# Performance work log

Measured on AMD Instinct MI355X. Metric: run time of the kernel, lower is better.

Reference implementation:

```python
import jax, jax.numpy as jnp
import numpy as np

NUM_ELMT = 64
INPUT_DIM = 16
BOUND = 50.0
MESH_RATIO = 1.2
N_POINTS = 1_048_576


def _build_mesh():
    m = NUM_ELMT
    one_step = BOUND * (MESH_RATIO - 1.0) / (MESH_RATIO ** (m / 2) - 1.0)
    idx = np.arange(-m / 2, m / 2 + 1)
    mesh = (MESH_RATIO ** np.abs(idx) - 1.0) / (MESH_RATIO - 1.0) * one_step * np.sign(idx)
    mesh_norm = (mesh + BOUND) / (2.0 * BOUND)
    mesh_norm = np.concatenate([[0.0], mesh_norm[1:-1], [1.0]]).astype(np.float32)
    elmt_size = (mesh_norm[1:] - mesh_norm[:-1]).astype(np.float32)
    return jnp.asarray(mesh_norm), jnp.asarray(elmt_size)


def setup_inputs() -> dict:
    key = jax.random.key(0)
    k1, k2 = jax.random.split(key)
    x = jax.random.uniform(k1, (N_POINTS, INPUT_DIM), jnp.float32, minval=-BOUND, maxval=BOUND)
    pdj = jnp.ones((N_POINTS, 1), jnp.float32)
    sldj = jnp.zeros((N_POINTS, 1), jnp.float32)
    log_p = 0.1 * jax.random.normal(k2, (NUM_ELMT - 1, INPUT_DIM), jnp.float32)
    mesh_norm, elmt_size = _build_mesh()
    return {"x": x, "pdj": pdj, "sldj": sldj, "log_p": log_p,
            "mesh_norm": mesh_norm, "elmt_size": elmt_size}


def _normalize_pdf(log_p, elmt_size):
    # elmt_size: (M,) -> (M,1) column, log_p: (M-1, D)
    es = elmt_size[:, None]
    ep = jnp.exp(log_p)
    px = ep * (es[:-1] + es[1:]) / 2.0
    px = ep * (1.0 - es[0]) / jnp.sum(px, axis=0, keepdims=True)
    p0 = jnp.ones((1, log_p.shape[1]), log_p.dtype)
    pdf_norm = jnp.concatenate([p0, px, p0], axis=0)            # (M+1, D)
    cell = (pdf_norm[:-1] + pdf_norm[1:]) / 2.0 * es            # (M, D)
    # F_ref[i] = sum(cell[:i]); single cumsum instead of the O(M^2) torch loop
    F_ref = jnp.concatenate([jnp.zeros_like(p0), jnp.cumsum(cell, axis=0)[:-1]], axis=0)  # (M, D)
    return pdf_norm, F_ref


def reference(x, pdj, sldj, log_p, mesh_norm, elmt_size):
    pdf_norm, F_ref = _normalize_pdf(log_p, elmt_size)
    xn = (x + BOUND) / (2.0 * BOUND)                            # (N, D) in [0,1]
    k = jnp.searchsorted(mesh_norm, xn, side='left')            # (N, D), torch right=False
    cover = (k != 0) & (k != NUM_ELMT + 1)
    k = jnp.clip(k, 1, NUM_ELMT)
    km1 = k - 1
    v1 = jnp.take_along_axis(pdf_norm, km1, axis=0)             # pdf at lower node
    v2 = jnp.take_along_axis(pdf_norm, k, axis=0)               # pdf at upper node
    xmodi = xn - mesh_norm[km1]                                 # offset inside element
    h = elmt_size[km1]                                          # element width
    F_pre = jnp.take_along_axis(F_ref, km1, axis=0)             # CDF at lower node
    y = jnp.where(cover, F_pre + xmodi * xmodi * 0.5 * (v2 - v1) / h + xmodi * v1, xn)
    abs_det = jnp.where(cover, xmodi * (v2 - v1) / h + v1, 1.0)
    pdj_out = pdj * jnp.prod(abs_det, axis=-1, keepdims=True)
    sldj_out = sldj + jnp.sum(jnp.log(abs_det), axis=-1, keepdims=True)
    x_out = y * 2.0 * BOUND - BOUND
    return (x_out, pdj_out, sldj_out)
```

## Files before the change

kernel.cpp:

```cpp
#include <hip/hip_runtime.h>
#include <math.h>


namespace {
constexpr int DIM = 16;
constexpr int ME  = 64;
constexpr float BOUNDF = 50.0f;
constexpr float K1      = 6.8164378f;
constexpr float INV_L2R = 3.8017840f;
constexpr int COEF_FLOATS = ME * 68;
constexpr int EP_BASE     = COEF_FLOATS - 63 * DIM;
}

__global__ __launch_bounds__(256) void nll_kernel(
    const float* __restrict__ x,
    const float* __restrict__ pdj,
    const float* __restrict__ sldj,
    const float* __restrict__ log_p,
    const float* __restrict__ mesh_norm,
    float* __restrict__ out,
    int npts, int npairs)
{
  __shared__ __align__(16) float co[COEF_FLOATS];
  __shared__ float s_mesh[ME + 1];

  const int tid = threadIdx.x;

  if (tid <= ME) s_mesh[tid] = mesh_norm[tid];
  for (int i = tid; i < 63 * DIM; i += 256)
    co[EP_BASE + i] = __expf(log_p[i]);
  __syncthreads();

  const int wv = tid >> 6, lane = tid & 63;
  float epv[4];
#pragma unroll
  for (int i = 0; i < 4; ++i)
    epv[i] = (lane < 63) ? co[EP_BASE + lane * DIM + (4 * wv + i)] : 0.f;
  const float mj  = s_mesh[lane];
  const float mj1 = s_mesh[lane + 1];
  const float mj2 = s_mesh[(lane + 2 > ME) ? ME : (lane + 2)];
  const float es0 = s_mesh[1] - s_mesh[0];
  __syncthreads();

  const float h = mj1 - mj;
#pragma unroll
  for (int i = 0; i < 4; ++i) {
    const int d = 4 * wv + i;
    const float ep = epv[i];
    float ss = (lane < 63) ? ep * (mj2 - mj) : 0.f;
    ss += __shfl_xor(ss, 1);  ss += __shfl_xor(ss, 2);  ss += __shfl_xor(ss, 4);
    ss += __shfl_xor(ss, 8);  ss += __shfl_xor(ss, 16); ss += __shfl_xor(ss, 32);
    const float scale = (1.0f - es0) / (0.5f * ss);
    const float cur = (lane < 63) ? ep * scale : 1.0f;
    float prev = __shfl_up(cur, 1);
    if (lane == 0) prev = 1.0f;
    const float cell = (prev + cur) * 0.5f * h;
    float v = cell, o;
    o = __shfl_up(v, 1);  if (lane >= 1)  v += o;
    o = __shfl_up(v, 2);  if (lane >= 2)  v += o;
    o = __shfl_up(v, 4);  if (lane >= 4)  v += o;
    o = __shfl_up(v, 8);  if (lane >= 8)  v += o;
    o = __shfl_up(v, 16); if (lane >= 16) v += o;
    o = __shfl_up(v, 32); if (lane >= 32) v += o;
    const float F = v - cell;
    const float A = 0.5f * (cur - prev) / h;
    const float B = fmaf(-(A + A), mj, prev);
    const float D = fmaf(mj, fmaf(mj, A, -prev), F);
    *reinterpret_cast<float4*>(&co[lane * 68 + 4 * d]) = make_float4(A, B, D, A + A);
  }
  __syncthreads();

  const int tpg = gridDim.x * blockDim.x;
  const float4* __restrict__ x4 = reinterpret_cast<const float4*>(x);
  float4* __restrict__ out4 = reinterpret_cast<float4*>(out);
  const int np16 = npts * DIM;

  for (int t = blockIdx.x * blockDim.x + tid; t < npairs; t += tpg) {
    const int p  = t >> 1;
    const int hh = t & 1;
    const float4 xa = x4[2 * t];
    const float4 xb = x4[2 * t + 1];
    const float ps = hh ? sldj[p] : pdj[p];
    const float vals[8] = {xa.x, xa.y, xa.z, xa.w, xb.x, xb.y, xb.z, xb.w};

    float xn[8];
    int   off[8];
#pragma unroll
    for (int j = 0; j < 8; ++j) {
      const float val = vals[j];
      xn[j] = (val + BOUNDF) * 0.01f;
      const float u = fmaf(fabsf(val), K1, 1.0f);
      const float n = __log2f(u) * INV_L2R;
      int km1 = 31 + (int)ceilf(copysignf(n, val));
      km1 = km1 < 0 ? 0 : (km1 > 63 ? 63 : km1);
      off[j] = km1 * 68 + (((hh << 3) + j) << 2);
    }

    float4 cf[8];
#pragma unroll
    for (int j = 0; j < 8; ++j)
      cf[j] = *reinterpret_cast<const float4*>(&co[off[j]]);

    float yv[8], dt[8];
#pragma unroll
    for (int j = 0; j < 8; ++j) {
      const float z = xn[j];
      float y = fmaf(z, fmaf(z, cf[j].x, cf[j].y), cf[j].z);
      float d = fmaf(z, cf[j].w, cf[j].y);
      const bool cover = (z > 0.f) && (z <= 1.0f);
      y = cover ? y : z;
      d = cover ? d : 1.0f;
      yv[j] = fmaf(y, 2.0f * BOUNDF, -BOUNDF);
      dt[j] = d;
    }
    const float prod = ((dt[0] * dt[1]) * (dt[2] * dt[3])) *
                       ((dt[4] * dt[5]) * (dt[6] * dt[7]));

    out4[2 * t]     = make_float4(yv[0], yv[1], yv[2], yv[3]);
    out4[2 * t + 1] = make_float4(yv[4], yv[5], yv[6], yv[7]);

    const float full = prod * __shfl_xor(prod, 1);
    const float res  = hh ? (ps + __logf(full)) : (ps * full);
    out[np16 + hh * npts + p] = res;
  }
}

extern "C" void kernel_launch(void* const* d_in, const int* in_sizes, int n_in,
                              void* d_out, int out_size, void* d_ws, size_t ws_size,
                              hipStream_t stream) {
  const float* x    = (const float*)d_in[0];
  const float* pdj  = (const float*)d_in[1];
  const float* sldj = (const float*)d_in[2];
  const float* lp   = (const float*)d_in[3];
  const float* mesh = (const float*)d_in[4];
  float* out = (float*)d_out;

  const int npts   = in_sizes[0] / DIM;
  const int npairs = npts * 2;
  const int block  = 256;
  int grid = 2048;
  const int needed = (npairs + block - 1) / block;
  if (needed < grid) grid = needed;

  hipLaunchKernelGGL(nll_kernel, dim3(grid), dim3(block), 0, stream,
                     x, pdj, sldj, lp, mesh, out, npts, npairs);
}
```

Baseline: 33.94 us.

## Prefetch two iterations ahead and fold out-of-range handling into sentinel bins

The grid-stride loop becomes a software pipeline that loads x and pdj/sldj two iterations ahead, so global-memory latency overlaps with the table lookups and arithmetic. The coefficient table gains two sentinel rows (A=0, B=1, D=0) for points below and above the mesh, which removes the per-element cover test and selects. This raises register pressure, which may lower occupancy. The sentinel rows also make points outside the mesh return z instead of passing through the cover branch.

```diff
diff --git a/kernel.cpp b/kernel.cpp
--- a/kernel.cpp
+++ b/kernel.cpp
@@ -1,5 +1,6 @@
 #include <hip/hip_runtime.h>
 #include <math.h>
+#include <stdint.h>
 
 
 namespace {
@@ -8,8 +9,10 @@
 constexpr float BOUNDF = 50.0f;
 constexpr float K1      = 6.8164378f;
 constexpr float INV_L2R = 3.8017840f;
-constexpr int COEF_FLOATS = ME * 68;
-constexpr int EP_BASE     = COEF_FLOATS - 63 * DIM;
+constexpr int NBIN = 66;
+constexpr int ROWF = 68;
+constexpr int COEF_FLOATS = NBIN * ROWF;
+constexpr int EP_BASE = COEF_FLOATS - 63 * DIM;
 }
 
 __global__ __launch_bounds__(256) void nll_kernel(
@@ -66,7 +69,12 @@
     const float A = 0.5f * (cur - prev) / h;
     const float B = fmaf(-(A + A), mj, prev);
     const float D = fmaf(mj, fmaf(mj, A, -prev), F);
-    *reinterpret_cast<float4*>(&co[lane * 68 + 4 * d]) = make_float4(A, B, D, A + A);
+    *reinterpret_cast<float4*>(&co[(lane + 1) * ROWF + 4 * d]) = make_float4(A, B, D, A + A);
+  }
+  if (tid < 32) {
+    const int row = (tid >> 4) ? (NBIN - 1) : 0;
+    const int d = tid & 15;
+    *reinterpret_cast<float4*>(&co[row * ROWF + 4 * d]) = make_float4(0.f, 1.f, 0.f, 0.f);
   }
   __syncthreads();
 
@@ -75,43 +83,57 @@
   float4* __restrict__ out4 = reinterpret_cast<float4*>(out);
   const int np16 = npts * DIM;
 
-  for (int t = blockIdx.x * blockDim.x + tid; t < npairs; t += tpg) {
+  int t = blockIdx.x * blockDim.x + tid;
+  if (t >= npairs) return;
+
+  float4 a0 = x4[2 * t], a1 = x4[2 * t + 1];
+  float aps = (t & 1) ? sldj[t >> 1] : pdj[t >> 1];
+  int tB = t + tpg;
+  bool hasB = tB < npairs;
+  float4 b0, b1; float bps = 0.f;
+  if (hasB) {
+    b0 = x4[2 * tB]; b1 = x4[2 * tB + 1];
+    bps = (tB & 1) ? sldj[tB >> 1] : pdj[tB >> 1];
+  }
+
+  while (true) {
+    const int tC = t + 2 * tpg;
+    const bool hasC = tC < npairs;
+    float4 c0, c1; float cps = 0.f;
+    if (hasC) {
+      c0 = x4[2 * tC]; c1 = x4[2 * tC + 1];
+      cps = (tC & 1) ? sldj[tC >> 1] : pdj[tC >> 1];
+    }
+
     const int p  = t >> 1;
     const int hh = t & 1;
-    const float4 xa = x4[2 * t];
-    const float4 xb = x4[2 * t + 1];
-    const float ps = hh ? sldj[p] : pdj[p];
-    const float vals[8] = {xa.x, xa.y, xa.z, xa.w, xb.x, xb.y, xb.z, xb.w};
+    const int dbase = hh << 5;
+    const float vals[8] = {a0.x, a0.y, a0.z, a0.w, a1.x, a1.y, a1.z, a1.w};
 
     float xn[8];
-    int   off[8];
+    int   idx[8];
 #pragma unroll
     for (int j = 0; j < 8; ++j) {
       const float val = vals[j];
-      xn[j] = (val + BOUNDF) * 0.01f;
+      xn[j] = fmaf(val, 0.01f, 0.5f);
       const float u = fmaf(fabsf(val), K1, 1.0f);
       const float n = __log2f(u) * INV_L2R;
-      int km1 = 31 + (int)ceilf(copysignf(n, val));
-      km1 = km1 < 0 ? 0 : (km1 > 63 ? 63 : km1);
-      off[j] = km1 * 68 + (((hh << 3) + j) << 2);
+      int k = 32 + (int)ceilf(copysignf(n, val));
+      k = k < 0 ? 0 : (k > NBIN - 1 ? NBIN - 1 : k);
+      idx[j] = k * ROWF + dbase + (j << 2);
     }
 
     float4 cf[8];
 #pragma unroll
     for (int j = 0; j < 8; ++j)
-      cf[j] = *reinterpret_cast<const float4*>(&co[off[j]]);
+      cf[j] = *reinterpret_cast<const float4*>(&co[idx[j]]);
 
     float yv[8], dt[8];
 #pragma unroll
     for (int j = 0; j < 8; ++j) {
       const float z = xn[j];
-      float y = fmaf(z, fmaf(z, cf[j].x, cf[j].y), cf[j].z);
-      float d = fmaf(z, cf[j].w, cf[j].y);
-      const bool cover = (z > 0.f) && (z <= 1.0f);
-      y = cover ? y : z;
-      d = cover ? d : 1.0f;
-      yv[j] = fmaf(y, 2.0f * BOUNDF, -BOUNDF);
-      dt[j] = d;
+      yv[j] = fmaf(fmaf(z, fmaf(z, cf[j].x, cf[j].y), cf[j].z), 2.0f * BOUNDF, -BOUNDF);
+      dt[j] = fmaf(z, cf[j].w, cf[j].y);
     }
     const float prod = ((dt[0] * dt[1]) * (dt[2] * dt[3])) *
                        ((dt[4] * dt[5]) * (dt[6] * dt[7]));
@@ -120,8 +142,12 @@
     out4[2 * t + 1] = make_float4(yv[4], yv[5], yv[6], yv[7]);
 
     const float full = prod * __shfl_xor(prod, 1);
-    const float res  = hh ? (ps + __logf(full)) : (ps * full);
+    const float res  = hh ? (aps + __logf(full)) : (aps * full);
     out[np16 + hh * npts + p] = res;
+
+    if (!hasB) break;
+    t = tB; a0 = b0; a1 = b1; aps = bps;
+    tB = tC; hasB = hasC; b0 = c0; b1 = c1; bps = cps;
   }
 }
 
```

After: 32.85 us. 1.03x faster.
